# Optimization experiments

Hardware: AMD Instinct MI355X
Metric: run time of the kernel (lower is better)

Reference implementation:

```python
import jax, jax.numpy as jnp
import numpy as np

D_MODEL = 512
EXPAND = 2
D_INNER = EXPAND * D_MODEL          # 1024
HEADDIM = 64
NHEADS = D_INNER // HEADDIM         # 16
D_STATE = 64
NGROUPS = 1
D_CONV = 7
D_FF = 2048
CONV_DIM = D_INNER + 2 * NGROUPS * D_STATE              # 1152
D_IN_PROJ = 2 * D_INNER + 2 * NGROUPS * D_STATE + 2 * NHEADS  # 2208
BATCH, SEQLEN = 4, 2048
EPS = 1e-5


def setup_inputs() -> dict:
    key = jax.random.key(0)
    ks = jax.random.split(key, 8)
    g = lambda k, shape, scale: jax.random.normal(k, shape, jnp.float32) * scale
    # dt_bias = inverse softplus of dt values in [1e-3, 0.1] (Mamba2 init convention)
    dt = jnp.linspace(1e-3, 0.1, NHEADS, dtype=jnp.float32)
    return {
        "x": jax.random.normal(ks[0], (BATCH, SEQLEN, D_MODEL), jnp.float32),
        "ln1_w": jnp.ones((D_MODEL,), jnp.float32),
        "ln1_b": jnp.zeros((D_MODEL,), jnp.float32),
        "in_proj_w": g(ks[1], (D_IN_PROJ, D_MODEL), 0.02),
        "conv_w": g(ks[2], (CONV_DIM, D_CONV), 0.2),
        "conv_b": jnp.zeros((CONV_DIM,), jnp.float32),
        "dt_bias": jnp.log(jnp.expm1(dt)),
        "A_log": jnp.log(jnp.arange(1, NHEADS + 1, dtype=jnp.float32)),
        "Dp": jnp.ones((NHEADS,), jnp.float32),
        "rms_w": jnp.ones((D_INNER,), jnp.float32),
        "out_proj_w": g(ks[3], (D_MODEL, D_INNER), 0.02),
        "ln2_w": jnp.ones((D_MODEL,), jnp.float32),
        "ln2_b": jnp.zeros((D_MODEL,), jnp.float32),
        "fc1_w": g(ks[4], (D_FF, D_MODEL), 0.02),
        "fc1_b": jnp.zeros((D_FF,), jnp.float32),
        "fc2_w": g(ks[5], (D_MODEL, D_FF), 0.02),
        "fc2_b": jnp.zeros((D_MODEL,), jnp.float32),
    }


def _layernorm(x, w, b):
    mu = jnp.mean(x, -1, keepdims=True)
    var = jnp.mean((x - mu) ** 2, -1, keepdims=True)
    return (x - mu) * jax.lax.rsqrt(var + EPS) * w + b


def _hydra(u, in_proj_w, conv_w, conv_b, dt_bias, A_log, Dp, rms_w, out_proj_w):
    B, L, _ = u.shape
    zxbcdt = u @ in_proj_w.T                                   # (B,L,D_IN_PROJ)
    z = zxbcdt[..., :D_INNER]                                  # gate
    xBC = zxbcdt[..., D_INNER:D_INNER + CONV_DIM]
    dt = zxbcdt[..., D_INNER + CONV_DIM:]                      # (B,L,2H)
    # forward / (time-reversed) backward dt, stacked on batch dim -> (2B,L,H)
    dt = jnp.concatenate([dt[..., :NHEADS], jnp.flip(dt[..., NHEADS:], axis=1)], axis=0)
    dt = jax.nn.softplus(dt + dt_bias)
    # depthwise causal conv1d (torch padding=d_conv-1 then [:, :L])
    xc = jax.lax.conv_general_dilated(
        jnp.transpose(xBC, (0, 2, 1)), conv_w[:, None, :],
        window_strides=(1,), padding=[(D_CONV - 1, 0)],
        feature_group_count=CONV_DIM, dimension_numbers=("NCH", "OIH", "NCH"))
    xBC = jax.nn.silu(jnp.transpose(xc, (0, 2, 1)) + conv_b)   # (B,L,CONV_DIM)
    xs = xBC[..., :D_INNER]
    Bm = xBC[..., D_INNER:D_INNER + NGROUPS * D_STATE]
    Cm = xBC[..., D_INNER + NGROUPS * D_STATE:]
    x_og = xs
    both = lambda a: jnp.concatenate([a, jnp.flip(a, axis=1)], axis=0)  # (2B,...)
    xs, Bm, Cm = both(xs), both(Bm), both(Cm)
    xh = xs.reshape(2 * B, L, NHEADS, HEADDIM)
    A = -jnp.exp(A_log)                                        # (H,) scalar-per-head SSD
    decay = jnp.exp(A * dt)                                    # (2B,L,H)
    dtx = dt[..., None] * xh                                   # (2B,L,H,P)

    def step(h, inp):
        dec_t, dtx_t, B_t, C_t = inp
        # h: (2B,H,P,N)
        h = h * dec_t[..., None, None] + dtx_t[..., None] * B_t[:, None, None, :]
        y = jnp.einsum("bhpn,bn->bhp", h, C_t)
        return h, y

    h0 = jnp.zeros((2 * B, NHEADS, HEADDIM, D_STATE), u.dtype)
    mv = lambda a: jnp.moveaxis(a, 1, 0)  # time-major for scan
    _, y = jax.lax.scan(step, h0, (mv(decay), mv(dtx), mv(Bm), mv(Cm)))
    y = jnp.moveaxis(y, 0, 1).reshape(2 * B, L, D_INNER)
    # shift by one (strictly off-diagonal quasiseparable parts)
    y = jnp.concatenate([jnp.zeros_like(y[:, :1]), y[:, :-1]], axis=1)
    y_fw, y_bw = y[:B], jnp.flip(y[B:], axis=1)
    y = y_fw + y_bw + x_og * jnp.repeat(Dp, HEADDIM)           # diagonal via D
    # gated RMSNorm then out projection
    yg = y * jax.nn.silu(z)
    yg = yg * jax.lax.rsqrt(jnp.mean(yg * yg, -1, keepdims=True) + EPS) * rms_w
    return yg @ out_proj_w.T


def reference(x, ln1_w, ln1_b, in_proj_w, conv_w, conv_b, dt_bias, A_log, Dp,
              rms_w, out_proj_w, ln2_w, ln2_b, fc1_w, fc1_b, fc2_w, fc2_b):
    # pre-norm Hydra block with residual (dropout = identity at eval)
    h = _layernorm(x, ln1_w, ln1_b)
    x = x + _hydra(h, in_proj_w, conv_w, conv_b, dt_bias, A_log, Dp, rms_w, out_proj_w)
    # FFN block with its own pre-norm + residual
    f = _layernorm(x, ln2_w, ln2_b)
    f = jax.nn.gelu(f @ fc1_w.T + fc1_b, approximate=False)
    f = f @ fc2_w.T + fc2_b
    return x + f
```

## Files before the change

kernel.cpp:

```cpp
#include <hip/hip_runtime.h>
#include <math.h>

#define D_MODEL   512
#define D_INNER   1024
#define NHEADS    16
#define HEADDIM   64
#define D_STATE   64
#define D_CONV    7
#define D_FF      2048
#define CONV_DIM  1152
#define D_IN_PROJ 2208
#define BATCH     4
#define SEQLEN    2048
#define NTOK      (BATCH*SEQLEN)
#define EPS       1e-5f

#define OFF_XBCB  9043968ull
#define OFF_XT    13762560ull
#define OFF_YFW   17956864ull
#define OFF_YBW   26345472ull
#define OFF_SREG  34734080ull

typedef __bf16 bf16x8 __attribute__((ext_vector_type(8)));
typedef float  f32x4  __attribute__((ext_vector_type(4)));

__device__ __forceinline__ float siluf(float x) { return x / (1.f + expf(-x)); }
__device__ __forceinline__ float geluf(float x) { return 0.5f * x * (1.f + erff(x * 0.70710678118654752f)); }
__device__ __forceinline__ float softplusf(float x) { return fmaxf(x, 0.f) + log1pf(expf(-fabsf(x))); }
__device__ __forceinline__ int tglob(int d, int c, int t) { int s = c * 64 + t; return d ? (SEQLEN - 1 - s) : s; }
__device__ __forceinline__ unsigned short f2bf(float f) {
    unsigned int u = __float_as_uint(f);
    u += 0x7FFFu + ((u >> 16) & 1u);
    return (unsigned short)(u >> 16);
}
__device__ __forceinline__ float bf2f(unsigned short u) { return __uint_as_float((unsigned)u << 16); }
__device__ __forceinline__ void glds16(const void* g, void* l) {
    __builtin_amdgcn_global_load_lds((const __attribute__((address_space(1))) void*)g,
                                     (__attribute__((address_space(3))) void*)l, 16, 0, 0);
}

__global__ __launch_bounds__(256) void ln_kernel(const float* __restrict__ x,
                                                 const float* __restrict__ w,
                                                 const float* __restrict__ b,
                                                 unsigned short* __restrict__ out, int nrows)
{
    int wid = threadIdx.x >> 6;
    int lane = threadIdx.x & 63;
    int row = blockIdx.x * 4 + wid;
    if (row >= nrows) return;
    const float* xr = x + (size_t)row * D_MODEL;
    float4 v0 = *(const float4*)(xr + lane * 8);
    float4 v1 = *(const float4*)(xr + lane * 8 + 4);
    float v[8] = {v0.x, v0.y, v0.z, v0.w, v1.x, v1.y, v1.z, v1.w};
    float s = 0.f;
#pragma unroll
    for (int i = 0; i < 8; i++) s += v[i];
#pragma unroll
    for (int m = 1; m < 64; m <<= 1) s += __shfl_xor(s, m, 64);
    float mu = s * (1.f / D_MODEL);
    float q = 0.f;
#pragma unroll
    for (int i = 0; i < 8; i++) { float dd = v[i] - mu; q += dd * dd; }
#pragma unroll
    for (int m = 1; m < 64; m <<= 1) q += __shfl_xor(q, m, 64);
    float inv = rsqrtf(q * (1.f / D_MODEL) + EPS);
    float4 w0 = *(const float4*)(w + lane * 8);
    float4 w1 = *(const float4*)(w + lane * 8 + 4);
    float4 b0 = *(const float4*)(b + lane * 8);
    float4 b1 = *(const float4*)(b + lane * 8 + 4);
    float o[8];
    o[0] = (v[0]-mu)*inv*w0.x + b0.x; o[1] = (v[1]-mu)*inv*w0.y + b0.y;
    o[2] = (v[2]-mu)*inv*w0.z + b0.z; o[3] = (v[3]-mu)*inv*w0.w + b0.w;
    o[4] = (v[4]-mu)*inv*w1.x + b1.x; o[5] = (v[5]-mu)*inv*w1.y + b1.y;
    o[6] = (v[6]-mu)*inv*w1.z + b1.z; o[7] = (v[7]-mu)*inv*w1.w + b1.w;
    unsigned short* orow = out + (size_t)row * D_MODEL + lane * 8;
    ushort4 p0, p1;
    p0.x = f2bf(o[0]); p0.y = f2bf(o[1]); p0.z = f2bf(o[2]); p0.w = f2bf(o[3]);
    p1.x = f2bf(o[4]); p1.y = f2bf(o[5]); p1.z = f2bf(o[6]); p1.w = f2bf(o[7]);
    *(ushort4*)orow = p0;
    *(ushort4*)(orow + 4) = p1;
}

__global__ __launch_bounds__(256) void wconv_kernel(const float* __restrict__ src,
                                                    unsigned short* __restrict__ dst,
                                                    int src_n, int dst_n)
{
    int i = (blockIdx.x * 256 + threadIdx.x) * 4;
    if (i >= dst_n) return;
    ushort4 o;
    if (i < src_n) {
        float4 v = *(const float4*)(src + i);
        o.x = f2bf(v.x); o.y = f2bf(v.y); o.z = f2bf(v.z); o.w = f2bf(v.w);
    } else {
        o.x = o.y = o.z = o.w = 0;
    }
    *(ushort4*)(dst + i) = o;
}

__global__ __launch_bounds__(256, 2) void gemm_bf16(const unsigned short* __restrict__ A,
                                                    const unsigned short* __restrict__ W,
                                                    int K, int Nreal,
                                                    float* __restrict__ Cf,
                                                    unsigned short* __restrict__ Cb,
                                                    const float* __restrict__ bias,
                                                    const float* __restrict__ res, int act,
                                                    float* __restrict__ dtf)
{
    __shared__ unsigned short As[128 * 32];
    __shared__ unsigned short Ws[128 * 32];
    const int tid = threadIdx.x;
    const int wave = tid >> 6;
    const int lane = tid & 63;
    const int m0 = blockIdx.x * 128;
    const int n0 = blockIdx.y * 128;
    const int wm = (wave & 1) * 64;
    const int wn = (wave >> 1) * 64;

    const size_t gA = (size_t)(m0 + 32 * wave + (lane >> 2)) * K + (lane & 3) * 8;
    const size_t gW = (size_t)(n0 + 32 * wave + (lane >> 2)) * K + (lane & 3) * 8;
    unsigned short* lA = As + wave * 1024 + lane * 8;
    unsigned short* lW = Ws + wave * 1024 + lane * 8;

    const int fr = lane & 15;
    const int fq = (lane >> 4) * 8;
    f32x4 acc[4][4] = {};

    for (int k0 = 0; k0 < K; k0 += 32) {
        glds16(A + gA + k0, lA);
        glds16(A + gA + (size_t)16 * K + k0, lA + 512);
        glds16(W + gW + k0, lW);
        glds16(W + gW + (size_t)16 * K + k0, lW + 512);
        __syncthreads();
        bf16x8 af[4], bf[4];
#pragma unroll
        for (int mi = 0; mi < 4; mi++)
            af[mi] = *(const bf16x8*)(As + (wm + mi * 16 + fr) * 32 + fq);
#pragma unroll
        for (int ni = 0; ni < 4; ni++)
            bf[ni] = *(const bf16x8*)(Ws + (wn + ni * 16 + fr) * 32 + fq);
#pragma unroll
        for (int mi = 0; mi < 4; mi++)
#pragma unroll
            for (int ni = 0; ni < 4; ni++)
                acc[mi][ni] = __builtin_amdgcn_mfma_f32_16x16x32_bf16(af[mi], bf[ni], acc[mi][ni], 0, 0, 0);
        __syncthreads();
    }

    const int colb = n0 + wn + (lane & 15);
    const int rowb = m0 + wm + (lane >> 4) * 4;
#pragma unroll
    for (int mi = 0; mi < 4; mi++) {
#pragma unroll
        for (int ni = 0; ni < 4; ni++) {
            int col = colb + ni * 16;
            if (col < Nreal) {
#pragma unroll
                for (int r = 0; r < 4; r++) {
                    int row = rowb + mi * 16 + r;
                    float v = acc[mi][ni][r];
                    size_t idx = (size_t)row * Nreal + col;
                    if (bias) v += bias[col];
                    if (res) v += res[idx];
                    if (act) v = geluf(v);
                    if (Cb) {
                        Cb[idx] = f2bf(v);
                        if (dtf && col >= 2176) dtf[(size_t)row * 32 + (col - 2176)] = v;
                    } else Cf[idx] = v;
                }
            }
        }
    }
}

__global__ __launch_bounds__(256) void gemm_bf16_t64(const unsigned short* __restrict__ A,
                                                     const unsigned short* __restrict__ W,
                                                     int K, int N,
                                                     float* __restrict__ Cf,
                                                     const float* __restrict__ bias,
                                                     const float* __restrict__ res)
{
    __shared__ unsigned short As[64 * 32];
    __shared__ unsigned short Ws[64 * 32];
    const int tid = threadIdx.x;
    const int wave = tid >> 6;
    const int lane = tid & 63;
    const int m0 = blockIdx.x * 64;
    const int n0 = blockIdx.y * 64;

    const size_t gA = (size_t)(m0 + (tid >> 2)) * K + (tid & 3) * 8;
    const size_t gW = (size_t)(n0 + (tid >> 2)) * K + (tid & 3) * 8;
    unsigned short* lA = As + tid * 8;
    unsigned short* lW = Ws + tid * 8;

    const int fr = lane & 15;
    const int fq = (lane >> 4) * 8;
    f32x4 acc[4] = {};

    for (int k0 = 0; k0 < K; k0 += 32) {
        glds16(A + gA + k0, lA);
        glds16(W + gW + k0, lW);
        __syncthreads();
        bf16x8 af = *(const bf16x8*)(As + (wave * 16 + fr) * 32 + fq);
#pragma unroll
        for (int ni = 0; ni < 4; ni++) {
            bf16x8 bfr = *(const bf16x8*)(Ws + (ni * 16 + fr) * 32 + fq);
            acc[ni] = __builtin_amdgcn_mfma_f32_16x16x32_bf16(af, bfr, acc[ni], 0, 0, 0);
        }
        __syncthreads();
    }

    const int col0 = n0 + (lane & 15);
    const int rowb = m0 + wave * 16 + (lane >> 4) * 4;
#pragma unroll
    for (int ni = 0; ni < 4; ni++) {
        int col = col0 + ni * 16;
        float bb = bias ? bias[col] : 0.f;
#pragma unroll
        for (int r = 0; r < 4; r++) {
            int row = rowb + r;
            size_t idx = (size_t)row * N + col;
            float v = acc[ni][r] + bb;
            if (res) v += res[idx];
            Cf[idx] = v;
        }
    }
}

__global__ __launch_bounds__(256) void conv_kernel(const unsigned short* __restrict__ zx,
                                                   const float* __restrict__ conv_w,
                                                   const float* __restrict__ conv_b,
                                                   unsigned short* __restrict__ out)
{
    int gid = blockIdx.x * 256 + threadIdx.x;
    int c4 = gid % 288;
    int tt = gid / 288;
    int c = c4 * 4;
    int b = tt >> 8;
    int t0 = (tt & 255) * 8;

    float wgt[4][7], bias[4];
#pragma unroll
    for (int q = 0; q < 4; q++) {
        bias[q] = conv_b[c + q];
#pragma unroll
        for (int j = 0; j < 7; j++) wgt[q][j] = conv_w[(c + q) * 7 + j];
    }

    float xin[4][14];
    const unsigned short* base = zx + (size_t)(b * SEQLEN + t0) * D_IN_PROJ + D_INNER + c;
#pragma unroll
    for (int j = 0; j < 14; j++) {
        int t = t0 - 6 + j;
        ushort4 v = make_ushort4(0, 0, 0, 0);
        if (t >= 0) v = *(const ushort4*)(base + (ptrdiff_t)(j - 6) * D_IN_PROJ);
        xin[0][j] = bf2f(v.x); xin[1][j] = bf2f(v.y);
        xin[2][j] = bf2f(v.z); xin[3][j] = bf2f(v.w);
    }

    unsigned short* orow = out + (size_t)(b * SEQLEN + t0) * CONV_DIM + c;
#pragma unroll
    for (int i = 0; i < 8; i++) {
        ushort4 o;
        float a0 = bias[0], a1 = bias[1], a2 = bias[2], a3 = bias[3];
#pragma unroll
        for (int j = 0; j < 7; j++) {
            a0 = fmaf(wgt[0][j], xin[0][i + j], a0);
            a1 = fmaf(wgt[1][j], xin[1][i + j], a1);
            a2 = fmaf(wgt[2][j], xin[2][i + j], a2);
            a3 = fmaf(wgt[3][j], xin[3][i + j], a3);
        }
        o.x = f2bf(siluf(a0)); o.y = f2bf(siluf(a1));
        o.z = f2bf(siluf(a2)); o.w = f2bf(siluf(a3));
        *(ushort4*)(orow + (size_t)i * CONV_DIM) = o;
    }
}

__global__ __launch_bounds__(256) void xpose_kernel(const unsigned short* __restrict__ xbc,
                                                    unsigned short* __restrict__ xT)
{
    int tt = blockIdx.x, pt = blockIdx.y, b = blockIdx.z;
    __shared__ unsigned short T[64][68];
    {
        int r = threadIdx.x >> 4, q = threadIdx.x & 15;
#pragma unroll
        for (int i = 0; i < 4; i++) {
            int t = tt * 64 + r + i * 16;
            ushort4 v = *(const ushort4*)(xbc + (size_t)(b * SEQLEN + t) * CONV_DIM + pt * 64 + q * 4);
            *(ushort4*)&T[r + i * 16][q * 4] = v;
        }
    }
    __syncthreads();
    {
        int p = threadIdx.x >> 4, tq = threadIdx.x & 15;
#pragma unroll
        for (int i = 0; i < 4; i++) {
            int pp = p + i * 16;
            ushort4 o;
            o.x = T[tq * 4 + 0][pp]; o.y = T[tq * 4 + 1][pp];
            o.z = T[tq * 4 + 2][pp]; o.w = T[tq * 4 + 3][pp];
            *(ushort4*)(xT + ((size_t)b * 1024 + pt * 64 + pp) * 2048 + tt * 64 + tq * 4) = o;
        }
    }
}

__global__ __launch_bounds__(256) void dt_table_kernel(const float* __restrict__ dtf,
                                                       const float* __restrict__ dt_bias,
                                                       const float* __restrict__ A_log,
                                                       float* __restrict__ cum_tab,
                                                       float* __restrict__ dtv_tab)
{
    int wid = blockIdx.x * 4 + (threadIdx.x >> 6);
    int lane = threadIdx.x & 63;
    int c = wid & 31, h = (wid >> 5) & 15, b = (wid >> 9) & 3, d = wid >> 11;
    int tg = tglob(d, c, lane);
    float raw = dtf[(size_t)(b * SEQLEN + tg) * 32 + d * 16 + h] + dt_bias[h];
    float dtv = softplusf(raw);
    float cum = -expf(A_log[h]) * dtv;
#pragma unroll
    for (int off = 1; off < 64; off <<= 1) {
        int src = lane - off;
        float o = __shfl(cum, src < 0 ? 0 : src, 64);
        if (lane >= off) cum += o;
    }
    cum_tab[(size_t)wid * 64 + lane] = cum;
    dtv_tab[(size_t)wid * 64 + lane] = dtv;
}

__global__ __launch_bounds__(256) void bzero_kernel(float* __restrict__ y_fw, float* __restrict__ y_bw)
{
    int b = blockIdx.x >> 1, d = blockIdx.x & 1;
    float* row = d ? (y_bw + (size_t)(b * SEQLEN + SEQLEN - 1) * D_INNER)
                   : (y_fw + (size_t)(b * SEQLEN) * D_INNER);
    *(float4*)(row + threadIdx.x * 4) = make_float4(0.f, 0.f, 0.f, 0.f);
}

__global__ __launch_bounds__(256) void ssd_intra_mfma(const unsigned short* __restrict__ xbc,
                                                      const unsigned short* __restrict__ xT,
                                                      const float* __restrict__ cum_tab,
                                                      const float* __restrict__ dtv_tab,
                                                      float* __restrict__ y_fw,
                                                      float* __restrict__ y_bw)
{
    const int bid = blockIdx.x;
    const int hq = bid & 3, c = (bid >> 2) & 31, b = (bid >> 7) & 3, d = bid >> 9;
    const int tid = threadIdx.x, wave = tid >> 6, lane = tid & 63;

    __shared__ unsigned short BnMt[64 * 80];
    __shared__ unsigned short CnXt[64 * 80];
    __shared__ float Gm[64 * 68];
    __shared__ float cum_l[64], dtv_l[64];

    {
        int s = tid >> 2, nq = (tid & 3) * 16;
        int tg = tglob(d, c, s);
        const unsigned short* row = xbc + (size_t)(b * SEQLEN + tg) * CONV_DIM;
#pragma unroll
        for (int k = 0; k < 16; k += 4) {
            *(ushort4*)&BnMt[s * 80 + nq + k] = *(const ushort4*)(row + 1024 + nq + k);
            *(ushort4*)&CnXt[s * 80 + nq + k] = *(const ushort4*)(row + 1088 + nq + k);
        }
    }
    __syncthreads();
    {
        f32x4 ga[4] = {};
        const int mrow = wave * 16 + (lane & 15);
        const int kq = (lane >> 4) * 8;
#pragma unroll
        for (int k0 = 0; k0 < 64; k0 += 32) {
            bf16x8 afr = *(const bf16x8*)&BnMt[mrow * 80 + k0 + kq];
#pragma unroll
            for (int ni = 0; ni < 4; ni++) {
                bf16x8 bfr = *(const bf16x8*)&CnXt[(ni * 16 + (lane & 15)) * 80 + k0 + kq];
                ga[ni] = __builtin_amdgcn_mfma_f32_16x16x32_bf16(afr, bfr, ga[ni], 0, 0, 0);
            }
        }
        int col = lane & 15, quad = lane >> 4;
#pragma unroll
        for (int ni = 0; ni < 4; ni++)
#pragma unroll
            for (int r = 0; r < 4; r++)
                Gm[(wave * 16 + quad * 4 + r) * 68 + ni * 16 + col] = ga[ni][r];
    }

    for (int hh = 0; hh < 4; hh++) {
        const int h = hq * 4 + hh;
        __syncthreads();
        if (tid < 64) {
            int flat = ((d * 4 + b) * 16 + h) * 32 + c;
            cum_l[tid] = cum_tab[(size_t)flat * 64 + tid];
            dtv_l[tid] = dtv_tab[(size_t)flat * 64 + tid];
        }
        {
            const unsigned short* xrow = xT + ((size_t)b * 1024 + h * 64) * 2048;
            int p = tid >> 4, tq = tid & 15;
#pragma unroll
            for (int pi = 0; pi < 4; pi++, p += 16) {
                if (d == 0) {
                    ushort4 v = *(const ushort4*)(xrow + (size_t)p * 2048 + c * 64 + tq * 4);
                    *(ushort4*)&CnXt[p * 80 + tq * 4] = v;
                } else {
                    int base = SEQLEN - 64 - c * 64;
                    ushort4 v = *(const ushort4*)(xrow + (size_t)p * 2048 + base + (15 - tq) * 4);
                    CnXt[p * 80 + tq * 4 + 0] = v.w;
                    CnXt[p * 80 + tq * 4 + 1] = v.z;
                    CnXt[p * 80 + tq * 4 + 2] = v.y;
                    CnXt[p * 80 + tq * 4 + 3] = v.x;
                }
            }
        }
        __syncthreads();
        {
            int s = tid & 63, tq = tid >> 6;
            float cs = cum_l[s], dv = dtv_l[s];
#pragma unroll
            for (int j = 0; j < 16; j++) {
                int t = tq * 16 + j;
                float g = Gm[s * 68 + t];
                float m = (s <= t) ? g * expf(cum_l[t] - cs) * dv : 0.f;
                BnMt[t * 80 + s] = f2bf(m);
            }
        }
        __syncthreads();
        {
            f32x4 acc[4] = {};
            const int mrow = wave * 16 + (lane & 15);
            const int kq = (lane >> 4) * 8;
#pragma unroll
            for (int k0 = 0; k0 < 64; k0 += 32) {
                bf16x8 afr = *(const bf16x8*)&BnMt[mrow * 80 + k0 + kq];
#pragma unroll
                for (int ni = 0; ni < 4; ni++) {
                    bf16x8 bfr = *(const bf16x8*)&CnXt[(ni * 16 + (lane & 15)) * 80 + k0 + kq];
                    acc[ni] = __builtin_amdgcn_mfma_f32_16x16x32_bf16(afr, bfr, acc[ni], 0, 0, 0);
                }
            }
            float* ybuf = d ? y_bw : y_fw;
            int quad = lane >> 4, col0 = lane & 15;
#pragma unroll
            for (int r = 0; r < 4; r++) {
                int tl = wave * 16 + quad * 4 + r;
                int tg = tglob(d, c, tl);
                int tout = d ? (tg - 1) : (tg + 1);
                if (tout >= 0 && tout < SEQLEN) {
                    float* yp = ybuf + (size_t)(b * SEQLEN + tout) * D_INNER + h * 64;
#pragma unroll
                    for (int ni = 0; ni < 4; ni++)
                        yp[ni * 16 + col0] = acc[ni][r];
                }
            }
        }
    }
}

__global__ __launch_bounds__(256) void ssd_state_kernel(const unsigned short* __restrict__ xbc,
                                                        const float* __restrict__ cum_tab,
                                                        const float* __restrict__ dtv_tab,
                                                        unsigned short* __restrict__ sreg16)
{
    const int flat = blockIdx.x;
    const int c = flat & 31, h = (flat >> 5) & 15, b = (flat >> 9) & 3, d = flat >> 11;
    const int tid = threadIdx.x;
    const int ty = tid >> 4, tx = tid & 15;

    __shared__ float Bm[64][64];
    __shared__ float Xw[64][64];
    __shared__ float cum_l[64], dtv_l[64];

    if (tid < 64) {
        cum_l[tid] = cum_tab[(size_t)flat * 64 + tid];
        dtv_l[tid] = dtv_tab[(size_t)flat * 64 + tid];
    }
    __syncthreads();
    float clast = cum_l[63];
    for (int idx = tid; idx < 1024; idx += 256) {
        int s = idx >> 4, q = idx & 15;
        int tg = tglob(d, c, s);
        const unsigned short* row = xbc + (size_t)(b * SEQLEN + tg) * CONV_DIM;
        ushort4 ub = *(const ushort4*)(row + 1024 + q * 4);
        ushort4 ux = *(const ushort4*)(row + h * 64 + q * 4);
        float w = expf(clast - cum_l[s]) * dtv_l[s];
        Bm[s][q*4+0] = bf2f(ub.x); Bm[s][q*4+1] = bf2f(ub.y);
        Bm[s][q*4+2] = bf2f(ub.z); Bm[s][q*4+3] = bf2f(ub.w);
        Xw[s][q*4+0] = bf2f(ux.x)*w; Xw[s][q*4+1] = bf2f(ux.y)*w;
        Xw[s][q*4+2] = bf2f(ux.z)*w; Xw[s][q*4+3] = bf2f(ux.w)*w;
    }
    __syncthreads();
    float acc[4][4] = {};
    for (int s = 0; s < 64; s++) {
        float4 xv = *(const float4*)&Xw[s][ty * 4];
        float4 bv = *(const float4*)&Bm[s][tx * 4];
        float xx[4] = {xv.x, xv.y, xv.z, xv.w};
        float bb[4] = {bv.x, bv.y, bv.z, bv.w};
#pragma unroll
        for (int i = 0; i < 4; i++)
#pragma unroll
            for (int j = 0; j < 4; j++) acc[i][j] = fmaf(xx[i], bb[j], acc[i][j]);
    }
    unsigned short* st = sreg16 + (size_t)flat * 4096;
#pragma unroll
    for (int i = 0; i < 4; i++) {
        ushort4 o;
        o.x = f2bf(acc[i][0]); o.y = f2bf(acc[i][1]);
        o.z = f2bf(acc[i][2]); o.w = f2bf(acc[i][3]);
        *(ushort4*)&st[(size_t)(ty * 4 + i) * 64 + tx * 4] = o;
    }
}

__global__ __launch_bounds__(256) void ssd_chunkscan_kernel(const float* __restrict__ cum_tab,
                                                            unsigned short* __restrict__ sreg16)
{
    const int ps = blockIdx.x & 3;
    const int g  = blockIdx.x >> 2;
    const int tid = threadIdx.x;
    const int base = g * 32;
    const size_t off = (size_t)ps * 1024 + tid * 4;
    float h0 = 0.f, h1 = 0.f, h2 = 0.f, h3 = 0.f;
    ushort4 s = *(ushort4*)(sreg16 + (size_t)base * 4096 + off);
    for (int c = 0; c < 32; c++) {
        int flat = base + c;
        ushort4 snext;
        if (c < 31) snext = *(ushort4*)(sreg16 + (size_t)(flat + 1) * 4096 + off);
        float dec = expf(cum_tab[(size_t)flat * 64 + 63]);
        ushort4 o;
        o.x = f2bf(h0); o.y = f2bf(h1); o.z = f2bf(h2); o.w = f2bf(h3);
        *(ushort4*)(sreg16 + (size_t)flat * 4096 + off) = o;
        h0 = h0 * dec + bf2f(s.x);
        h1 = h1 * dec + bf2f(s.y);
        h2 = h2 * dec + bf2f(s.z);
        h3 = h3 * dec + bf2f(s.w);
        s = snext;
    }
}

__global__ __launch_bounds__(256) void ssd_inter_mfma(const unsigned short* __restrict__ xbc,
                                                      const float* __restrict__ cum_tab,
                                                      const unsigned short* __restrict__ sreg16,
                                                      float* __restrict__ y_fw,
                                                      float* __restrict__ y_bw)
{
    const int flat = blockIdx.x;
    const int c = flat & 31;
    if (c == 0) return;
    const int h = (flat >> 5) & 15, b = (flat >> 9) & 3, d = flat >> 11;
    const int tid = threadIdx.x, wave = tid >> 6, lane = tid & 63;

    __shared__ unsigned short Cs[64 * 72];
    __shared__ unsigned short Hs[64 * 72];
    __shared__ float cum_l[64];

    if (tid < 64) cum_l[tid] = cum_tab[(size_t)flat * 64 + tid];
    {
        int s = tid >> 2, nq = (tid & 3) * 16;
        int tg = tglob(d, c, s);
        const unsigned short* row = xbc + (size_t)(b * SEQLEN + tg) * CONV_DIM + 1088;
        const unsigned short* st = sreg16 + (size_t)flat * 4096 + s * 64;
#pragma unroll
        for (int k = 0; k < 16; k += 4) {
            *(ushort4*)&Cs[s * 72 + nq + k] = *(const ushort4*)(row + nq + k);
            *(ushort4*)&Hs[s * 72 + nq + k] = *(const ushort4*)(st + nq + k);
        }
    }
    __syncthreads();
    f32x4 acc[4] = {};
    const int fr = lane & 15, kq = (lane >> 4) * 8;
    const int mrow = wave * 16 + fr;
#pragma unroll
    for (int k0 = 0; k0 < 64; k0 += 32) {
        bf16x8 afr = *(const bf16x8*)&Cs[mrow * 72 + k0 + kq];
#pragma unroll
        for (int ni = 0; ni < 4; ni++) {
            bf16x8 bfr = *(const bf16x8*)&Hs[(ni * 16 + fr) * 72 + k0 + kq];
            acc[ni] = __builtin_amdgcn_mfma_f32_16x16x32_bf16(afr, bfr, acc[ni], 0, 0, 0);
        }
    }
    float* ybuf = d ? y_bw : y_fw;
    int quad = lane >> 4, col0 = lane & 15;
#pragma unroll
    for (int r = 0; r < 4; r++) {
        int tl = wave * 16 + quad * 4 + r;
        float a = expf(cum_l[tl]);
        int tg = tglob(d, c, tl);
        int tout = d ? (tg - 1) : (tg + 1);
        if (tout >= 0 && tout < SEQLEN) {
            float* yp = ybuf + (size_t)(b * SEQLEN + tout) * D_INNER + h * 64;
#pragma unroll
            for (int ni = 0; ni < 4; ni++)
                yp[ni * 16 + col0] += acc[ni][r] * a;
        }
    }
}

__global__ __launch_bounds__(256) void combine_kernel(const unsigned short* __restrict__ zx,
                                                      const unsigned short* __restrict__ xbc,
                                                      const float* __restrict__ y_fw,
                                                      const float* __restrict__ y_bw,
                                                      const float* __restrict__ Dp,
                                                      const float* __restrict__ rms_w,
                                                      unsigned short* __restrict__ yg)
{
    int row = blockIdx.x;
    int i = threadIdx.x * 4;
    float4 yf = *(const float4*)(y_fw + (size_t)row * D_INNER + i);
    float4 yb = *(const float4*)(y_bw + (size_t)row * D_INNER + i);
    ushort4 uxs = *(const ushort4*)(xbc + (size_t)row * CONV_DIM + i);
    ushort4 uz  = *(const ushort4*)(zx + (size_t)row * D_IN_PROJ + i);
    float dp = Dp[i >> 6];
    float g[4];
    g[0] = (yf.x + yb.x + bf2f(uxs.x) * dp) * siluf(bf2f(uz.x));
    g[1] = (yf.y + yb.y + bf2f(uxs.y) * dp) * siluf(bf2f(uz.y));
    g[2] = (yf.z + yb.z + bf2f(uxs.z) * dp) * siluf(bf2f(uz.z));
    g[3] = (yf.w + yb.w + bf2f(uxs.w) * dp) * siluf(bf2f(uz.w));
    float ss = g[0]*g[0] + g[1]*g[1] + g[2]*g[2] + g[3]*g[3];
#pragma unroll
    for (int m = 1; m < 64; m <<= 1) ss += __shfl_xor(ss, m, 64);
    __shared__ float red[4];
    if ((threadIdx.x & 63) == 0) red[threadIdx.x >> 6] = ss;
    __syncthreads();
    ss = red[0] + red[1] + red[2] + red[3];
    float scale = rsqrtf(ss * (1.f / D_INNER) + EPS);
    float4 rw = *(const float4*)(rms_w + i);
    ushort4 o;
    o.x = f2bf(g[0] * scale * rw.x); o.y = f2bf(g[1] * scale * rw.y);
    o.z = f2bf(g[2] * scale * rw.z); o.w = f2bf(g[3] * scale * rw.w);
    *(ushort4*)(yg + (size_t)row * D_INNER + i) = o;
}

extern "C" void kernel_launch(void* const* d_in, const int* in_sizes, int n_in,
                              void* d_out, int out_size, void* d_ws, size_t ws_size,
                              hipStream_t stream)
{
    const float* x         = (const float*)d_in[0];
    const float* ln1_w     = (const float*)d_in[1];
    const float* ln1_b     = (const float*)d_in[2];
    const float* in_proj_w = (const float*)d_in[3];
    const float* conv_w    = (const float*)d_in[4];
    const float* conv_b    = (const float*)d_in[5];
    const float* dt_bias   = (const float*)d_in[6];
    const float* A_log     = (const float*)d_in[7];
    const float* Dp        = (const float*)d_in[8];
    const float* rms_w     = (const float*)d_in[9];
    const float* out_proj_w= (const float*)d_in[10];
    const float* ln2_w     = (const float*)d_in[11];
    const float* ln2_b     = (const float*)d_in[12];
    const float* fc1_w     = (const float*)d_in[13];
    const float* fc1_b     = (const float*)d_in[14];
    const float* fc2_w     = (const float*)d_in[15];
    const float* fc2_b     = (const float*)d_in[16];
    float* out = (float*)d_out;

    float* ws0 = (float*)d_ws;
    unsigned short* zx_bf  = (unsigned short*)ws0;
    unsigned short* xbc_bf = (unsigned short*)(ws0 + OFF_XBCB);
    unsigned short* xT_bf  = (unsigned short*)(ws0 + OFF_XT);
    float* y_fw = ws0 + OFF_YFW;
    float* y_bw = ws0 + OFF_YBW;
    float* sreg = ws0 + OFF_SREG;
    unsigned short* sreg16 = (unsigned short*)sreg;
    unsigned short* hA_bf = (unsigned short*)sreg;
    unsigned short* yg_bf = (unsigned short*)(sreg + 2686976);
    float* x_res          = sreg + 6881280;
    unsigned short* sh    = (unsigned short*)sreg;
    unsigned short* P_in  = sh + 22151168;
    unsigned short* P_out = sh + 23330816;
    unsigned short* P_f1  = sh + 23855104;
    unsigned short* P_f2  = sh + 24903680;
    unsigned short* f1_bf = (unsigned short*)ws0;
    float* cum_tab = out;
    float* dtv_tab = out + 262144;
    float* dtf     = out + 524288;

    wconv_kernel<<<dim3(2304 * 512 / 1024), dim3(256), 0, stream>>>(in_proj_w, P_in, 2208 * 512, 2304 * 512);
    wconv_kernel<<<dim3(512 * 1024 / 1024), dim3(256), 0, stream>>>(out_proj_w, P_out, 512 * 1024, 512 * 1024);
    wconv_kernel<<<dim3(2048 * 512 / 1024), dim3(256), 0, stream>>>(fc1_w, P_f1, 2048 * 512, 2048 * 512);
    wconv_kernel<<<dim3(512 * 2048 / 1024), dim3(256), 0, stream>>>(fc2_w, P_f2, 512 * 2048, 512 * 2048);
    ln_kernel<<<dim3(NTOK / 4), dim3(256), 0, stream>>>(x, ln1_w, ln1_b, hA_bf, NTOK);
    gemm_bf16<<<dim3(64, 18), dim3(256), 0, stream>>>(hA_bf, P_in, 512, 2208, nullptr, zx_bf, nullptr, nullptr, 0, dtf);
    conv_kernel<<<dim3(288 * 1024 / 256), dim3(256), 0, stream>>>(zx_bf, conv_w, conv_b, xbc_bf);
    xpose_kernel<<<dim3(32, 16, 4), dim3(256), 0, stream>>>(xbc_bf, xT_bf);
    dt_table_kernel<<<dim3(1024), dim3(256), 0, stream>>>(dtf, dt_bias, A_log, cum_tab, dtv_tab);
    bzero_kernel<<<dim3(8), dim3(256), 0, stream>>>(y_fw, y_bw);
    ssd_intra_mfma<<<dim3(1024), dim3(256), 0, stream>>>(xbc_bf, xT_bf, cum_tab, dtv_tab, y_fw, y_bw);
    ssd_state_kernel<<<dim3(4096), dim3(256), 0, stream>>>(xbc_bf, cum_tab, dtv_tab, sreg16);
    ssd_chunkscan_kernel<<<dim3(512), dim3(256), 0, stream>>>(cum_tab, sreg16);
    ssd_inter_mfma<<<dim3(4096), dim3(256), 0, stream>>>(xbc_bf, cum_tab, sreg16, y_fw, y_bw);
    combine_kernel<<<dim3(NTOK), dim3(256), 0, stream>>>(zx_bf, xbc_bf, y_fw, y_bw, Dp, rms_w, yg_bf);
    gemm_bf16_t64<<<dim3(128, 8), dim3(256), 0, stream>>>(yg_bf, P_out, 1024, 512, x_res, nullptr, x);
    ln_kernel<<<dim3(NTOK / 4), dim3(256), 0, stream>>>(x_res, ln2_w, ln2_b, hA_bf, NTOK);
    gemm_bf16<<<dim3(64, 16), dim3(256), 0, stream>>>(hA_bf, P_f1, 512, 2048, nullptr, f1_bf, fc1_b, nullptr, 1, nullptr);
    gemm_bf16_t64<<<dim3(128, 8), dim3(256), 0, stream>>>(f1_bf, P_f2, 2048, 512, out, fc2_b, x_res);
}
```

Measured before the change: 414.6 us.

## Merge weight conversion launches, fold y zeroing into SSD, widen GEMM K-step

The four fp32-to-bf16 weight conversion launches become a single kernel that picks its source and destination by index range. The separate kernel that zeroes the boundary rows of y_fw and y_bw is removed, and that zeroing now happens inside ssd_intra_mfma for chunk 0. Both GEMM kernels now stage 64 K-elements per barrier pair using two 32-wide LDS slices, halving the number of synchronisations. This doubles shared-memory use per block and raises register pressure, which could lower occupancy.

```diff
diff --git a/kernel.cpp b/kernel.cpp
--- a/kernel.cpp
+++ b/kernel.cpp
@@ -81,20 +81,23 @@
     *(ushort4*)(orow + 4) = p1;
 }
 
-__global__ __launch_bounds__(256) void wconv_kernel(const float* __restrict__ src,
-                                                    unsigned short* __restrict__ dst,
-                                                    int src_n, int dst_n)
-{
-    int i = (blockIdx.x * 256 + threadIdx.x) * 4;
-    if (i >= dst_n) return;
-    ushort4 o;
-    if (i < src_n) {
-        float4 v = *(const float4*)(src + i);
+__global__ __launch_bounds__(256) void wconv_all(const float* __restrict__ w0, unsigned short* __restrict__ p0,
+                                                 const float* __restrict__ w1, unsigned short* __restrict__ p1,
+                                                 const float* __restrict__ w2, unsigned short* __restrict__ p2,
+                                                 const float* __restrict__ w3, unsigned short* __restrict__ p3)
+{
+    int i = blockIdx.x * 256 + threadIdx.x;
+    const float* src; unsigned short* dst; int srcn;
+    if (i < 294912)      { src = w0; dst = p0; srcn = 282624; }
+    else if (i < 425984) { i -= 294912; src = w1; dst = p1; srcn = 131072; }
+    else if (i < 688128) { i -= 425984; src = w2; dst = p2; srcn = 262144; }
+    else                 { i -= 688128; src = w3; dst = p3; srcn = 262144; }
+    ushort4 o = make_ushort4(0, 0, 0, 0);
+    if (i < srcn) {
+        float4 v = ((const float4*)src)[i];
         o.x = f2bf(v.x); o.y = f2bf(v.y); o.z = f2bf(v.z); o.w = f2bf(v.w);
-    } else {
-        o.x = o.y = o.z = o.w = 0;
-    }
-    *(ushort4*)(dst + i) = o;
+    }
+    ((ushort4*)dst)[i] = o;
 }
 
 __global__ __launch_bounds__(256, 2) void gemm_bf16(const unsigned short* __restrict__ A,
@@ -106,8 +109,8 @@
                                                     const float* __restrict__ res, int act,
                                                     float* __restrict__ dtf)
 {
-    __shared__ unsigned short As[128 * 32];
-    __shared__ unsigned short Ws[128 * 32];
+    __shared__ unsigned short As[2][128 * 32];
+    __shared__ unsigned short Ws[2][128 * 32];
     const int tid = threadIdx.x;
     const int wave = tid >> 6;
     const int lane = tid & 63;
@@ -118,31 +121,37 @@
 
     const size_t gA = (size_t)(m0 + 32 * wave + (lane >> 2)) * K + (lane & 3) * 8;
     const size_t gW = (size_t)(n0 + 32 * wave + (lane >> 2)) * K + (lane & 3) * 8;
-    unsigned short* lA = As + wave * 1024 + lane * 8;
-    unsigned short* lW = Ws + wave * 1024 + lane * 8;
+    const int lofs = wave * 1024 + lane * 8;
 
     const int fr = lane & 15;
     const int fq = (lane >> 4) * 8;
     f32x4 acc[4][4] = {};
 
-    for (int k0 = 0; k0 < K; k0 += 32) {
-        glds16(A + gA + k0, lA);
-        glds16(A + gA + (size_t)16 * K + k0, lA + 512);
-        glds16(W + gW + k0, lW);
-        glds16(W + gW + (size_t)16 * K + k0, lW + 512);
+    for (int k0 = 0; k0 < K; k0 += 64) {
+        glds16(A + gA + k0, As[0] + lofs);
+        glds16(A + gA + (size_t)16 * K + k0, As[0] + lofs + 512);
+        glds16(A + gA + k0 + 32, As[1] + lofs);
+        glds16(A + gA + (size_t)16 * K + k0 + 32, As[1] + lofs + 512);
+        glds16(W + gW + k0, Ws[0] + lofs);
+        glds16(W + gW + (size_t)16 * K + k0, Ws[0] + lofs + 512);
+        glds16(W + gW + k0 + 32, Ws[1] + lofs);
+        glds16(W + gW + (size_t)16 * K + k0 + 32, Ws[1] + lofs + 512);
         __syncthreads();
-        bf16x8 af[4], bf[4];
-#pragma unroll
-        for (int mi = 0; mi < 4; mi++)
-            af[mi] = *(const bf16x8*)(As + (wm + mi * 16 + fr) * 32 + fq);
-#pragma unroll
-        for (int ni = 0; ni < 4; ni++)
-            bf[ni] = *(const bf16x8*)(Ws + (wn + ni * 16 + fr) * 32 + fq);
-#pragma unroll
-        for (int mi = 0; mi < 4; mi++)
+#pragma unroll
+        for (int p = 0; p < 2; p++) {
+            bf16x8 af[4], bf[4];
+#pragma unroll
+            for (int mi = 0; mi < 4; mi++)
+                af[mi] = *(const bf16x8*)(As[p] + (wm + mi * 16 + fr) * 32 + fq);
 #pragma unroll
             for (int ni = 0; ni < 4; ni++)
-                acc[mi][ni] = __builtin_amdgcn_mfma_f32_16x16x32_bf16(af[mi], bf[ni], acc[mi][ni], 0, 0, 0);
+                bf[ni] = *(const bf16x8*)(Ws[p] + (wn + ni * 16 + fr) * 32 + fq);
+#pragma unroll
+            for (int mi = 0; mi < 4; mi++)
+#pragma unroll
+                for (int ni = 0; ni < 4; ni++)
+                    acc[mi][ni] = __builtin_amdgcn_mfma_f32_16x16x32_bf16(af[mi], bf[ni], acc[mi][ni], 0, 0, 0);
+        }
         __syncthreads();
     }
 
@@ -179,8 +188,8 @@
                                                      const float* __restrict__ bias,
                                                      const float* __restrict__ res)
 {
-    __shared__ unsigned short As[64 * 32];
-    __shared__ unsigned short Ws[64 * 32];
+    __shared__ unsigned short As[2][64 * 32];
+    __shared__ unsigned short Ws[2][64 * 32];
     const int tid = threadIdx.x;
     const int wave = tid >> 6;
     const int lane = tid & 63;
@@ -189,22 +198,26 @@
 
     const size_t gA = (size_t)(m0 + (tid >> 2)) * K + (tid & 3) * 8;
     const size_t gW = (size_t)(n0 + (tid >> 2)) * K + (tid & 3) * 8;
-    unsigned short* lA = As + tid * 8;
-    unsigned short* lW = Ws + tid * 8;
+    const int lofs = tid * 8;
 
     const int fr = lane & 15;
     const int fq = (lane >> 4) * 8;
     f32x4 acc[4] = {};
 
-    for (int k0 = 0; k0 < K; k0 += 32) {
-        glds16(A + gA + k0, lA);
-        glds16(W + gW + k0, lW);
+    for (int k0 = 0; k0 < K; k0 += 64) {
+        glds16(A + gA + k0, As[0] + lofs);
+        glds16(A + gA + k0 + 32, As[1] + lofs);
+        glds16(W + gW + k0, Ws[0] + lofs);
+        glds16(W + gW + k0 + 32, Ws[1] + lofs);
         __syncthreads();
-        bf16x8 af = *(const bf16x8*)(As + (wave * 16 + fr) * 32 + fq);
-#pragma unroll
-        for (int ni = 0; ni < 4; ni++) {
-            bf16x8 bfr = *(const bf16x8*)(Ws + (ni * 16 + fr) * 32 + fq);
-            acc[ni] = __builtin_amdgcn_mfma_f32_16x16x32_bf16(af, bfr, acc[ni], 0, 0, 0);
+#pragma unroll
+        for (int p = 0; p < 2; p++) {
+            bf16x8 af = *(const bf16x8*)(As[p] + (wave * 16 + fr) * 32 + fq);
+#pragma unroll
+            for (int ni = 0; ni < 4; ni++) {
+                bf16x8 bfr = *(const bf16x8*)(Ws[p] + (ni * 16 + fr) * 32 + fq);
+                acc[ni] = __builtin_amdgcn_mfma_f32_16x16x32_bf16(af, bfr, acc[ni], 0, 0, 0);
+            }
         }
         __syncthreads();
     }
@@ -326,14 +339,6 @@
     dtv_tab[(size_t)wid * 64 + lane] = dtv;
 }
 
-__global__ __launch_bounds__(256) void bzero_kernel(float* __restrict__ y_fw, float* __restrict__ y_bw)
-{
-    int b = blockIdx.x >> 1, d = blockIdx.x & 1;
-    float* row = d ? (y_bw + (size_t)(b * SEQLEN + SEQLEN - 1) * D_INNER)
-                   : (y_fw + (size_t)(b * SEQLEN) * D_INNER);
-    *(float4*)(row + threadIdx.x * 4) = make_float4(0.f, 0.f, 0.f, 0.f);
-}
-
 __global__ __launch_bounds__(256) void ssd_intra_mfma(const unsigned short* __restrict__ xbc,
                                                       const unsigned short* __restrict__ xT,
                                                       const float* __restrict__ cum_tab,
@@ -350,6 +355,11 @@
     __shared__ float Gm[64 * 68];
     __shared__ float cum_l[64], dtv_l[64];
 
+    if (c == 0) {
+        int t0 = d ? (SEQLEN - 1) : 0;
+        float* ybuf = d ? y_bw : y_fw;
+        ybuf[(size_t)(b * SEQLEN + t0) * D_INNER + hq * 256 + tid] = 0.f;
+    }
     {
         int s = tid >> 2, nq = (tid & 3) * 16;
         int tg = tglob(d, c, s);
@@ -669,16 +679,12 @@
     float* dtv_tab = out + 262144;
     float* dtf     = out + 524288;
 
-    wconv_kernel<<<dim3(2304 * 512 / 1024), dim3(256), 0, stream>>>(in_proj_w, P_in, 2208 * 512, 2304 * 512);
-    wconv_kernel<<<dim3(512 * 1024 / 1024), dim3(256), 0, stream>>>(out_proj_w, P_out, 512 * 1024, 512 * 1024);
-    wconv_kernel<<<dim3(2048 * 512 / 1024), dim3(256), 0, stream>>>(fc1_w, P_f1, 2048 * 512, 2048 * 512);
-    wconv_kernel<<<dim3(512 * 2048 / 1024), dim3(256), 0, stream>>>(fc2_w, P_f2, 512 * 2048, 512 * 2048);
+    wconv_all<<<dim3(3712), dim3(256), 0, stream>>>(in_proj_w, P_in, out_proj_w, P_out, fc1_w, P_f1, fc2_w, P_f2);
     ln_kernel<<<dim3(NTOK / 4), dim3(256), 0, stream>>>(x, ln1_w, ln1_b, hA_bf, NTOK);
     gemm_bf16<<<dim3(64, 18), dim3(256), 0, stream>>>(hA_bf, P_in, 512, 2208, nullptr, zx_bf, nullptr, nullptr, 0, dtf);
     conv_kernel<<<dim3(288 * 1024 / 256), dim3(256), 0, stream>>>(zx_bf, conv_w, conv_b, xbc_bf);
     xpose_kernel<<<dim3(32, 16, 4), dim3(256), 0, stream>>>(xbc_bf, xT_bf);
     dt_table_kernel<<<dim3(1024), dim3(256), 0, stream>>>(dtf, dt_bias, A_log, cum_tab, dtv_tab);
-    bzero_kernel<<<dim3(8), dim3(256), 0, stream>>>(y_fw, y_bw);
     ssd_intra_mfma<<<dim3(1024), dim3(256), 0, stream>>>(xbc_bf, xT_bf, cum_tab, dtv_tab, y_fw, y_bw);
     ssd_state_kernel<<<dim3(4096), dim3(256), 0, stream>>>(xbc_bf, cum_tab, dtv_tab, sreg16);
     ssd_chunkscan_kernel<<<dim3(512), dim3(256), 0, stream>>>(cum_tab, sreg16);
```

After: 397.6 us. -4.1%, faster.
